# Performance work log

Hardware: AMD Instinct MI355X
Metric: run time of the kernel (lower is better)

## Reference

```python
import jax, jax.numpy as jnp
import numpy as np

B, T, D, H, O = 1024, 512, 64, 64, 32


def setup_inputs() -> dict:
    key = jax.random.key(0)
    ks = jax.random.split(key, 12)
    s = 1.0 / np.sqrt(H)  # torch LSTM/Linear default init scale
    u = lambda k, shape: jax.random.uniform(k, shape, jnp.float32, -s, s)
    return {
        "x": jax.random.normal(ks[0], (B, T, D), jnp.float32),
        # layer 0 (PyTorch gate order: i, f, g, o stacked along first dim)
        "w_ih0": u(ks[1], (4 * H, D)),
        "w_hh0": u(ks[2], (4 * H, H)),
        "b_ih0": u(ks[3], (4 * H,)),
        "b_hh0": u(ks[4], (4 * H,)),
        # layer 1
        "w_ih1": u(ks[5], (4 * H, H)),
        "w_hh1": u(ks[6], (4 * H, H)),
        "b_ih1": u(ks[7], (4 * H,)),
        "b_hh1": u(ks[8], (4 * H,)),
        # final linear head
        "fc_w": u(ks[9], (O, H)),
        "fc_b": u(ks[10], (O,)),
    }


def lstm_layer(x, w_ih, w_hh, b_ih, b_hh):
    """Single batch-first LSTM layer, PyTorch gate order (i, f, g, o)."""
    Bb = x.shape[0]
    Hh = w_hh.shape[1]
    # precompute input contribution for all timesteps: (B, T, 4H)
    pre = jnp.einsum('btd,gd->btg', x, w_ih) + b_ih + b_hh

    def step(carry, p_t):  # p_t: (B, 4H)
        h, c = carry
        gates = p_t + h @ w_hh.T
        i, f, g, o = jnp.split(gates, 4, axis=-1)
        c = jax.nn.sigmoid(f) * c + jax.nn.sigmoid(i) * jnp.tanh(g)
        h = jax.nn.sigmoid(o) * jnp.tanh(c)
        return (h, c), h

    h0 = jnp.zeros((Bb, Hh), x.dtype)
    (_, _), hs = jax.lax.scan(step, (h0, h0), jnp.swapaxes(pre, 0, 1))
    return jnp.swapaxes(hs, 0, 1)  # (B, T, H)


def reference(x, w_ih0, w_hh0, b_ih0, b_hh0, w_ih1, w_hh1, b_ih1, b_hh1, fc_w, fc_b):
    h1 = lstm_layer(x, w_ih0, w_hh0, b_ih0, b_hh0)
    h2 = lstm_layer(h1, w_ih1, w_hh1, b_ih1, b_hh1)
    last = h2[:, -1, :]  # (B, H)
    return jax.nn.softplus(last @ fc_w.T + fc_b)  # (B, O)
```

## Files before the change

### kernel.cpp

```cpp
#include <hip/hip_runtime.h>
#include <math.h>

#define BB 1024
#define TT 512
#define OO 32
#define MM 4
#define NBLK (BB/MM)
#define SS 8
#define NSLOT 66

typedef __attribute__((ext_vector_type(8))) short short8;
typedef __attribute__((ext_vector_type(4))) float f32x4;

#define MFMA __builtin_amdgcn_mfma_f32_16x16x32_bf16
#define LOG2E 1.4426950408889634f
#define K2    2.8853900817779268f

#define BAR() asm volatile("s_waitcnt lgkmcnt(0)\n\ts_barrier" ::: "memory")

__device__ __forceinline__ float exp2f_(float x) {
#if __has_builtin(__builtin_amdgcn_exp2f)
    return __builtin_amdgcn_exp2f(x);
#else
    float r; asm("v_exp_f32 %0, %1" : "=v"(r) : "v"(x)); return r;
#endif
}

__device__ __forceinline__ ushort f2bf(float f) {
    union { float f; unsigned u; } v; v.f = f;
    unsigned r = v.u + 0x7FFF + ((v.u >> 16) & 1);
    return (ushort)(r >> 16);
}
__device__ __forceinline__ float bf2f(ushort u) {
    union { unsigned u; float f; } v; v.u = ((unsigned)u) << 16; return v.f;
}
__device__ __forceinline__ unsigned pkbf(float a, float b) {
    union { float f; unsigned u; } x, y; x.f = a; y.f = b;
    return __builtin_amdgcn_perm(y.u + 0x8000u, x.u + 0x8000u, 0x07060302u);
}
__device__ __forceinline__ short8 pack8(const float4& a, const float4& b) {
    union { unsigned u[4]; short8 s; } r;
    r.u[0] = pkbf(a.x, a.y); r.u[1] = pkbf(a.z, a.w);
    r.u[2] = pkbf(b.x, b.y); r.u[3] = pkbf(b.z, b.w);
    return r.s;
}

__global__ __launch_bounds__(256, 1)
void lstm_pc(const float* __restrict__ x,
             const float* __restrict__ w_ih0,
             const float* __restrict__ w_hh0,
             const float* __restrict__ b_ih0,
             const float* __restrict__ b_hh0,
             const float* __restrict__ w_ih1,
             const float* __restrict__ w_hh1,
             const float* __restrict__ b_ih1,
             const float* __restrict__ b_hh1,
             const float* __restrict__ fc_w,
             const float* __restrict__ fc_b,
             float* __restrict__ out)
{
    __shared__ float  pre0[2][SS][4][4][64];
    __shared__ float  pre1[2][SS][4][4][64];
    __shared__ ushort h0u[16][4][80];
    __shared__ ushort h1u[2][4][80];

    const int tid = threadIdx.x;
    const int wv  = tid >> 6;
    const int ln  = tid & 63;
    const int l   = ln & 15;
    const int q   = ln >> 4;
    const int b0  = blockIdx.x * MM;
    const f32x4 z4 = (f32x4){0.f, 0.f, 0.f, 0.f};

    for (int i = tid; i < 16 * 4 * 80; i += 256) ((ushort*)h0u)[i] = 0;
    for (int i = tid; i < 2 * 4 * 80;  i += 256) ((ushort*)h1u)[i] = 0;

    if (wv < 2) {
        const float* whh = wv ? w_hh1 : w_hh0;
        short8 bf[4][4][2];
#pragma unroll
        for (int g = 0; g < 4; ++g) {
            const float sc = (g == 2) ? K2 : -LOG2E;
#pragma unroll
            for (int c = 0; c < 4; ++c) {
                const int col = 64 * g + 16 * c + l;
#pragma unroll
                for (int kt = 0; kt < 2; ++kt) {
                    const float* src = whh + col * 64 + 32 * kt + 8 * q;
                    const float4 v0 = *(const float4*)src;
                    const float4 v1 = *(const float4*)(src + 4);
                    short8 b;
                    b[0] = (short)f2bf(v0.x * sc); b[1] = (short)f2bf(v0.y * sc);
                    b[2] = (short)f2bf(v0.z * sc); b[3] = (short)f2bf(v0.w * sc);
                    b[4] = (short)f2bf(v1.x * sc); b[5] = (short)f2bf(v1.y * sc);
                    b[6] = (short)f2bf(v1.z * sc); b[7] = (short)f2bf(v1.w * sc);
                    bf[g][c][kt] = b;
                }
            }
        }
        float cc[4] = {0.f, 0.f, 0.f, 0.f};
        const int hrow = l >> 2;
        const int hsw  = (16 * q) ^ (16 * hrow);
        const float* preBase = wv ? &pre1[0][0][0][0][0] : &pre0[0][0][0][0][0];
        char* ring = (char*)(wv ? (void*)h1u : (void*)h0u);
        const int mask = wv ? 1 : 15;

        for (int s = 0; s < NSLOT; ++s) {
            BAR();
            const bool act = wv ? (s >= 2) : (s < 64);
            if (act) {
                const int u_  = wv ? (s - 2) : s;
                const int base_t = SS * u_;
                const float* pb0 = preBase + (u_ & 1) * 8192 + q * 256;
#pragma unroll
                for (int tau = 0; tau < SS; ++tau) {
                    const int t = base_t + tau;
                    const char* hb = ring + ((t - 1) & mask) * 640 + hrow * 160;
                    const short8 a0 = *(const short8*)(hb + hsw);
                    const short8 a1 = *(const short8*)(hb + 64 + hsw);
                    const float* pp = pb0 + tau * 1024;
                    float y[4][4];
#pragma unroll
                    for (int g = 0; g < 4; ++g)
#pragma unroll
                        for (int w = 0; w < 4; ++w)
                            y[g][w] = pp[g * 64 + ((16 * w + l) ^ (16 * q))];
#pragma unroll
                    for (int c = 0; c < 4; ++c)
#pragma unroll
                        for (int g = 0; g < 4; ++g) {
                            f32x4 acc = MFMA(a1, bf[g][c][1],
                                             MFMA(a0, bf[g][c][0], z4, 0, 0, 0),
                                             0, 0, 0);
                            y[g][c] += acc[0];
                        }
                    char* wb = ring + (t & mask) * 640 + q * 160;
#pragma unroll
                    for (int w = 0; w < 4; ++w) {
                        const float y0 = y[0][w], y1 = y[1][w];
                        const float y2 = y[2][w], y3 = y[3][w];
                        const float Ef = exp2f_(y1);
                        const float Ei = exp2f_(y0);
                        const float Eg = exp2f_(fminf(y2, 80.f));
                        const float sf = __builtin_amdgcn_rcpf(1.f + Ef);
                        const float rd = __builtin_amdgcn_rcpf((1.f + Ei) * (1.f + Eg));
                        cc[w] = sf * cc[w] + (Eg - 1.f) * rd;
                        const float Ec = exp2f_(fminf(cc[w] * K2, 80.f));
                        const float Eo = exp2f_(y3);
                        const float r2 = __builtin_amdgcn_rcpf((1.f + Eo) * (1.f + Ec));
                        union { float f; unsigned u; } hv; hv.f = (Ec - 1.f) * r2;
                        const ushort hval = (ushort)((hv.u + 0x8000u) >> 16);
                        *(ushort*)(wb + ((32 * w + 2 * l) ^ (16 * q))) = hval;
                    }
                }
            }
        }
    } else {
        const int c0 = 2 * (wv - 2);
        short8 wi0[4][2][2], wi1[4][2][2];
        float  bv0[4][2], bv1[4][2];
#pragma unroll
        for (int g = 0; g < 4; ++g) {
            const float sc = (g == 2) ? K2 : -LOG2E;
#pragma unroll
            for (int ci = 0; ci < 2; ++ci) {
                const int col = 64 * g + 16 * (c0 + ci) + l;
                bv0[g][ci] = (b_ih0[col] + b_hh0[col]) * sc;
                bv1[g][ci] = (b_ih1[col] + b_hh1[col]) * sc;
#pragma unroll
                for (int kt = 0; kt < 2; ++kt) {
                    const int ko = 32 * kt + 8 * q;
#define LDW(dst, W)                                                           \
                    { const float4 v0 = *(const float4*)(W + col * 64 + ko);  \
                      const float4 v1 = *(const float4*)(W + col * 64 + ko + 4); \
                      short8 b;                                               \
                      b[0]=(short)f2bf(v0.x*sc); b[1]=(short)f2bf(v0.y*sc);   \
                      b[2]=(short)f2bf(v0.z*sc); b[3]=(short)f2bf(v0.w*sc);   \
                      b[4]=(short)f2bf(v1.x*sc); b[5]=(short)f2bf(v1.y*sc);   \
                      b[6]=(short)f2bf(v1.z*sc); b[7]=(short)f2bf(v1.w*sc);   \
                      dst = b; }
                    LDW(wi0[g][ci][kt], w_ih0)
                    LDW(wi1[g][ci][kt], w_ih1)
#undef LDW
                }
            }
        }
        const int xrow = l & 3, xtau = l >> 2;
        const size_t xbase = ((size_t)(b0 + xrow) * TT) * 64 + 8 * q;

#define COOP_PRE0(S_)                                                         \
        {                                                                     \
            const int buf = ((S_) + 1) & 1;                                   \
            const int t0 = SS * ((S_) + 1);                                   \
            float* dst0 = &pre0[buf][0][0][0][0];                             \
            _Pragma("unroll")                                                 \
            for (int hh = 0; hh < 2; ++hh) {                                  \
                const float* px = x + xbase + (size_t)(t0 + 4 * hh + xtau) * 64; \
                const float4 v0 = *(const float4*)px;                         \
                const float4 v1 = *(const float4*)(px + 4);                   \
                const float4 v2 = *(const float4*)(px + 32);                  \
                const float4 v3 = *(const float4*)(px + 36);                  \
                const short8 xa0 = pack8(v0, v1), xa1 = pack8(v2, v3);        \
                _Pragma("unroll")                                             \
                for (int ci = 0; ci < 2; ++ci)                                \
                    _Pragma("unroll")                                         \
                    for (int g = 0; g < 4; ++g) {                             \
                        const float bv_ = bv0[g][ci];                         \
                        f32x4 acc = (f32x4){bv_, bv_, bv_, bv_};              \
                        acc = MFMA(xa0, wi0[g][ci][0], acc, 0, 0, 0);         \
                        acc = MFMA(xa1, wi0[g][ci][1], acc, 0, 0, 0);         \
                        const int uu = 16 * (c0 + ci) + l;                    \
                        float* dd = dst0 + (4 * hh + q) * 1024 + g * 64;      \
                        dd[0 * 256 + (uu ^ 0)]  = acc[0];                     \
                        dd[1 * 256 + (uu ^ 16)] = acc[1];                     \
                        dd[2 * 256 + (uu ^ 32)] = acc[2];                     \
                        dd[3 * 256 + (uu ^ 48)] = acc[3];                     \
                    }                                                         \
            }                                                                 \
        }

#define COOP_PRE1(S_)                                                         \
        {                                                                     \
            const int buf = ((S_) - 1) & 1;                                   \
            const int t1 = SS * ((S_) - 1);                                   \
            float* dst1 = &pre1[buf][0][0][0][0];                             \
            const int sw2 = (16 * q) ^ (16 * xrow);                           \
            _Pragma("unroll")                                                 \
            for (int hh = 0; hh < 2; ++hh) {                                  \
                const int tt = t1 + 4 * hh + xtau;                            \
                const char* hp = (const char*)h0u + (tt & 15) * 640 + xrow * 160; \
                const short8 ha0 = *(const short8*)(hp + sw2);                \
                const short8 ha1 = *(const short8*)(hp + 64 + sw2);           \
                _Pragma("unroll")                                             \
                for (int ci = 0; ci < 2; ++ci)                                \
                    _Pragma("unroll")                                         \
                    for (int g = 0; g < 4; ++g) {                             \
                        const float bv_ = bv1[g][ci];                         \
                        f32x4 acc = (f32x4){bv_, bv_, bv_, bv_};              \
                        acc = MFMA(ha0, wi1[g][ci][0], acc, 0, 0, 0);         \
                        acc = MFMA(ha1, wi1[g][ci][1], acc, 0, 0, 0);         \
                        const int uu = 16 * (c0 + ci) + l;                    \
                        float* dd = dst1 + (4 * hh + q) * 1024 + g * 64;      \
                        dd[0 * 256 + (uu ^ 0)]  = acc[0];                     \
                        dd[1 * 256 + (uu ^ 16)] = acc[1];                     \
                        dd[2 * 256 + (uu ^ 32)] = acc[2];                     \
                        dd[3 * 256 + (uu ^ 48)] = acc[3];                     \
                    }                                                         \
            }                                                                 \
        }

        COOP_PRE0(-1)
        for (int s = 0; s < NSLOT; ++s) {
            BAR();
            if (s < 63) COOP_PRE0(s)
            if (s >= 1 && s <= 64) COOP_PRE1(s)
        }
#undef COOP_PRE0
#undef COOP_PRE1
    }

    BAR();
    if (tid < MM * OO) {
        const int row = tid >> 5, o = tid & 31;
        float a = fc_b[o];
#pragma unroll
        for (int j = 0; j < 64; ++j) {
            const ushort hv = *(const ushort*)((const char*)h1u + 640
                              + row * 160 + ((2 * j) ^ (16 * row)));
            a = fmaf(fc_w[o * 64 + j], bf2f(hv), a);
        }
        out[(size_t)(b0 + row) * OO + o] =
            fmaxf(a, 0.0f) + log1pf(__expf(-fabsf(a)));
    }
}

extern "C" void kernel_launch(void* const* d_in, const int* in_sizes, int n_in,
                              void* d_out, int out_size, void* d_ws, size_t ws_size,
                              hipStream_t stream) {
    const float* x     = (const float*)d_in[0];
    const float* w_ih0 = (const float*)d_in[1];
    const float* w_hh0 = (const float*)d_in[2];
    const float* b_ih0 = (const float*)d_in[3];
    const float* b_hh0 = (const float*)d_in[4];
    const float* w_ih1 = (const float*)d_in[5];
    const float* w_hh1 = (const float*)d_in[6];
    const float* b_ih1 = (const float*)d_in[7];
    const float* b_hh1 = (const float*)d_in[8];
    const float* fc_w  = (const float*)d_in[9];
    const float* fc_b  = (const float*)d_in[10];
    float* out = (float*)d_out;

    lstm_pc<<<dim3(NBLK), dim3(256), 0, stream>>>(
        x, w_ih0, w_hh0, b_ih0, b_hh0,
        w_ih1, w_hh1, b_ih1, b_hh1, fc_w, fc_b, out);
}
```

Before: 472.9 us.

## Split each LSTM layer's recurrence across two waves and interleave input projections

Reworks the wave specialisation. Before, one wave per layer ran the whole recurrence while two waves computed the input projections. Now each layer's recurrent step is split across two waves (half the hidden columns each), and all four waves share the projection work, spread across the per-timestep tau slots. x is staged into LDS with asynchronous global_load_lds, and the pre-activation and hidden-state LDS layouts are changed for vector reads. This shortens the serial per-step critical path, at the cost of a workgroup barrier on every timestep instead of every 8 steps.

```diff
diff --git a/kernel.cpp b/kernel.cpp
--- a/kernel.cpp
+++ b/kernel.cpp
@@ -16,7 +16,8 @@
 #define LOG2E 1.4426950408889634f
 #define K2    2.8853900817779268f
 
-#define BAR() asm volatile("s_waitcnt lgkmcnt(0)\n\ts_barrier" ::: "memory")
+#define BAR()  asm volatile("s_waitcnt lgkmcnt(0)\n\ts_barrier" ::: "memory")
+#define BARV() asm volatile("s_waitcnt vmcnt(0) lgkmcnt(0)\n\ts_barrier" ::: "memory")
 
 __device__ __forceinline__ float exp2f_(float x) {
 #if __has_builtin(__builtin_amdgcn_exp2f)
@@ -45,8 +46,14 @@
     return r.s;
 }
 
+__device__ __forceinline__ void gll16(const float* g, void* l) {
+    __builtin_amdgcn_global_load_lds(
+        (const __attribute__((address_space(1))) void*)g,
+        (__attribute__((address_space(3))) void*)l, 16, 0, 0);
+}
+
 __global__ __launch_bounds__(256, 1)
-void lstm_pc(const float* __restrict__ x,
+void lstm_tw(const float* __restrict__ x,
              const float* __restrict__ w_ih0,
              const float* __restrict__ w_hh0,
              const float* __restrict__ b_ih0,
@@ -59,205 +66,259 @@
              const float* __restrict__ fc_b,
              float* __restrict__ out)
 {
-    __shared__ float  pre0[2][SS][4][4][64];
-    __shared__ float  pre1[2][SS][4][4][64];
-    __shared__ ushort h0u[16][4][80];
-    __shared__ ushort h1u[2][4][80];
+    __shared__ __align__(16) float  pre0s[2][SS][64][4][4];
+    __shared__ __align__(16) float  pre1s[2][SS][64][4][4];
+    __shared__ __align__(16) ushort h0s[16][4][64];
+    __shared__ __align__(16) ushort h1s[2][4][64];
+    __shared__ __align__(16) float  xs[2][4][SS][64];
 
     const int tid = threadIdx.x;
     const int wv  = tid >> 6;
+    const int lay = wv >> 1;
+    const int cA  = 2 * (wv & 1);
     const int ln  = tid & 63;
     const int l   = ln & 15;
     const int q   = ln >> 4;
     const int b0  = blockIdx.x * MM;
     const f32x4 z4 = (f32x4){0.f, 0.f, 0.f, 0.f};
 
-    for (int i = tid; i < 16 * 4 * 80; i += 256) ((ushort*)h0u)[i] = 0;
-    for (int i = tid; i < 2 * 4 * 80;  i += 256) ((ushort*)h1u)[i] = 0;
-
-    if (wv < 2) {
-        const float* whh = wv ? w_hh1 : w_hh0;
-        short8 bf[4][4][2];
-#pragma unroll
-        for (int g = 0; g < 4; ++g) {
-            const float sc = (g == 2) ? K2 : -LOG2E;
-#pragma unroll
-            for (int c = 0; c < 4; ++c) {
-                const int col = 64 * g + 16 * c + l;
-#pragma unroll
-                for (int kt = 0; kt < 2; ++kt) {
-                    const float* src = whh + col * 64 + 32 * kt + 8 * q;
-                    const float4 v0 = *(const float4*)src;
-                    const float4 v1 = *(const float4*)(src + 4);
-                    short8 b;
-                    b[0] = (short)f2bf(v0.x * sc); b[1] = (short)f2bf(v0.y * sc);
-                    b[2] = (short)f2bf(v0.z * sc); b[3] = (short)f2bf(v0.w * sc);
-                    b[4] = (short)f2bf(v1.x * sc); b[5] = (short)f2bf(v1.y * sc);
-                    b[6] = (short)f2bf(v1.z * sc); b[7] = (short)f2bf(v1.w * sc);
-                    bf[g][c][kt] = b;
-                }
-            }
-        }
-        float cc[4] = {0.f, 0.f, 0.f, 0.f};
-        const int hrow = l >> 2;
-        const int hsw  = (16 * q) ^ (16 * hrow);
-        const float* preBase = wv ? &pre1[0][0][0][0][0] : &pre0[0][0][0][0][0];
-        char* ring = (char*)(wv ? (void*)h1u : (void*)h0u);
-        const int mask = wv ? 1 : 15;
-
-        for (int s = 0; s < NSLOT; ++s) {
-            BAR();
-            const bool act = wv ? (s >= 2) : (s < 64);
-            if (act) {
-                const int u_  = wv ? (s - 2) : s;
-                const int base_t = SS * u_;
-                const float* pb0 = preBase + (u_ & 1) * 8192 + q * 256;
-#pragma unroll
-                for (int tau = 0; tau < SS; ++tau) {
-                    const int t = base_t + tau;
-                    const char* hb = ring + ((t - 1) & mask) * 640 + hrow * 160;
-                    const short8 a0 = *(const short8*)(hb + hsw);
-                    const short8 a1 = *(const short8*)(hb + 64 + hsw);
-                    const float* pp = pb0 + tau * 1024;
-                    float y[4][4];
+    const float* whh = lay ? w_hh1 : w_hh0;
+    short8 bf[4][2][2];
+#pragma unroll
+    for (int g = 0; g < 4; ++g) {
+        const float sc = (g == 2) ? K2 : -LOG2E;
+#pragma unroll
+        for (int ci = 0; ci < 2; ++ci) {
+            const int col = 64 * g + 16 * (cA + ci) + l;
+#pragma unroll
+            for (int kt = 0; kt < 2; ++kt) {
+                const float* src = whh + col * 64 + 32 * kt + 8 * q;
+                const float4 v0 = *(const float4*)src;
+                const float4 v1 = *(const float4*)(src + 4);
+                short8 b;
+                b[0] = (short)f2bf(v0.x * sc); b[1] = (short)f2bf(v0.y * sc);
+                b[2] = (short)f2bf(v0.z * sc); b[3] = (short)f2bf(v0.w * sc);
+                b[4] = (short)f2bf(v1.x * sc); b[5] = (short)f2bf(v1.y * sc);
+                b[6] = (short)f2bf(v1.z * sc); b[7] = (short)f2bf(v1.w * sc);
+                bf[g][ci][kt] = b;
+            }
+        }
+    }
+
+    const float scw = (wv == 2) ? K2 : -LOG2E;
+    short8 wi0[4][2], wi1[4][2];
+    float  bv0[4], bv1[4];
+#pragma unroll
+    for (int j = 0; j < 4; ++j) {
+        const int col = 64 * wv + 16 * j + l;
+        bv0[j] = (b_ih0[col] + b_hh0[col]) * scw;
+        bv1[j] = (b_ih1[col] + b_hh1[col]) * scw;
+#pragma unroll
+        for (int kt = 0; kt < 2; ++kt) {
+            const int ko = 32 * kt + 8 * q;
+#define LDW(dst, W)                                                           \
+            { const float4 v0 = *(const float4*)(W + col * 64 + ko);          \
+              const float4 v1 = *(const float4*)(W + col * 64 + ko + 4);      \
+              short8 b;                                                       \
+              b[0]=(short)f2bf(v0.x*scw); b[1]=(short)f2bf(v0.y*scw);         \
+              b[2]=(short)f2bf(v0.z*scw); b[3]=(short)f2bf(v0.w*scw);         \
+              b[4]=(short)f2bf(v1.x*scw); b[5]=(short)f2bf(v1.y*scw);         \
+              b[6]=(short)f2bf(v1.z*scw); b[7]=(short)f2bf(v1.w*scw);         \
+              dst = b; }
+            LDW(wi0[j][kt], w_ih0)
+            LDW(wi1[j][kt], w_ih1)
+#undef LDW
+        }
+    }
+
+    for (int i = tid; i < 16 * 4 * 64; i += 256) ((ushort*)h0s)[i] = 0;
+    for (int i = tid; i < 2 * 4 * 64;  i += 256) ((ushort*)h1s)[i] = 0;
+
+#pragma unroll
+    for (int c = 0; c < 2; ++c)
+#pragma unroll
+        for (int k = 0; k < 2; ++k) {
+            const int th = 4 * k;
+            const float* sr = x + (((size_t)(b0 + wv) * TT + 8 * c + th + (ln >> 4)) * 64
+                                   + (ln & 15) * 4);
+            gll16(sr, (char*)xs + c * 8192 + wv * 2048 + th * 256);
+        }
+    BARV();
+    {
+#pragma unroll
+        for (int mt = 0; mt < 2; ++mt) {
+            const float* xp = (const float*)xs + (l & 3) * 512
+                              + ((l >> 2) + 4 * mt) * 64 + 8 * q;
+            const float4 v0 = *(const float4*)xp;
+            const float4 v1 = *(const float4*)(xp + 4);
+            const float4 v2 = *(const float4*)(xp + 32);
+            const float4 v3 = *(const float4*)(xp + 36);
+            const short8 xa0 = pack8(v0, v1);
+            const short8 xa1 = pack8(v2, v3);
+            char* wp = (char*)pre0s + (q + 4 * mt) * 4096;
+#pragma unroll
+            for (int j = 0; j < 4; ++j) {
+                f32x4 a = (f32x4){bv0[j], bv0[j], bv0[j], bv0[j]};
+                a = MFMA(xa0, wi0[j][0], a, 0, 0, 0);
+                a = MFMA(xa1, wi0[j][1], a, 0, 0, 0);
+                char* wpp = wp + (16 * j + l) * 64 + wv * 4;
+#pragma unroll
+                for (int ri = 0; ri < 4; ++ri)
+                    *(float*)(wpp + ((ri * 16) ^ (q << 4))) = a[ri];
+            }
+        }
+    }
+    BAR();
+
+    float cc0 = 0.f, cc1 = 0.f;
+
+#define CELL(CCV, Y0, Y1, Y2, Y3, HVAL)                                       \
+    {                                                                         \
+        const float Ef = exp2f_(Y1);                                          \
+        const float Ei = exp2f_(Y0);                                          \
+        const float Eg = exp2f_(fminf((Y2), 80.f));                           \
+        const float sf = __builtin_amdgcn_rcpf(1.f + Ef);                     \
+        const float rd = __builtin_amdgcn_rcpf((1.f + Ei) * (1.f + Eg));      \
+        CCV = sf * CCV + (Eg - 1.f) * rd;                                     \
+        const float Ec = exp2f_(fminf(CCV * K2, 80.f));                       \
+        const float Eo = exp2f_(Y3);                                          \
+        const float r2 = __builtin_amdgcn_rcpf((1.f + Eo) * (1.f + Ec));      \
+        union { float f; unsigned u; } hv_; hv_.f = (Ec - 1.f) * r2;          \
+        HVAL = (ushort)((hv_.u + 0x8000u) >> 16);                             \
+    }
+
+    for (int s = 0; s < NSLOT; ++s) {
+        const int pb   = s & 1;
+        const bool doA = (lay == 0) && (s < 64);
+        const bool doB = (lay == 1) && (s >= 2);
+        const bool cp0 = (s <= 62);
+        const bool cp1 = (s >= 1 && s <= 64);
+        const int t0   = doA ? (8 * s) : (8 * (s - 2));
+        const int t1C  = 8 * (s - 1);
+        short8 ca0 = {0,0,0,0,0,0,0,0}, ca1 = {0,0,0,0,0,0,0,0};
+
+#pragma unroll
+        for (int tau = 0; tau < SS; ++tau) {
+            if (tau == 0) { BARV(); } else { BAR(); }
+
+            short8 a0, a1; f32x4 pv0, pv1;
+            if (doA || doB) {
+                const int t  = t0 + tau;
+                const int hm = doA ? 15 : 1;
+                const int r  = l >> 2;
+                const char* hb = (doA ? (const char*)h0s : (const char*)h1s)
+                                 + ((t - 1) & hm) * 512 + r * 128;
+                a0 = *(const short8*)(hb + ((16 * q) ^ (r << 4)));
+                a1 = *(const short8*)(hb + ((64 + 16 * q) ^ (r << 4)));
+                const char* pr = (doA ? (const char*)pre0s : (const char*)pre1s)
+                                 + pb * 16384 + tau * 4096
+                                 + ((16 * q) ^ ((tau & 3) << 4));
+                pv0 = *(const f32x4*)(pr + (16 * cA + l) * 64);
+                pv1 = *(const f32x4*)(pr + (16 * cA + 16 + l) * 64);
+            }
+
+            if (tau == 0 && s <= 61) {
+                const int sg = s + 2;
+                char* xd = (char*)xs + (sg & 1) * 8192 + wv * 2048;
+#pragma unroll
+                for (int k = 0; k < 2; ++k) {
+                    const int th = 4 * k;
+                    const float* sr = x + (((size_t)(b0 + wv) * TT + 8 * sg + th
+                                            + (ln >> 4)) * 64 + (ln & 15) * 4);
+                    gll16(sr, xd + th * 256);
+                }
+            }
+
+            if (tau < 4) {
+                if (cp0) {
+                    const int mt = tau >> 1;
+                    if ((tau & 1) == 0) {
+                        const float* xp = (const float*)xs + (pb ^ 1) * 2048
+                                          + (l & 3) * 512
+                                          + ((l >> 2) + 4 * mt) * 64 + 8 * q;
+                        const float4 v0 = *(const float4*)xp;
+                        const float4 v1 = *(const float4*)(xp + 4);
+                        const float4 v2 = *(const float4*)(xp + 32);
+                        const float4 v3 = *(const float4*)(xp + 36);
+                        ca0 = pack8(v0, v1); ca1 = pack8(v2, v3);
+                    }
+                    const int j0 = 2 * (tau & 1);
+                    char* wp = (char*)pre0s + (pb ^ 1) * 16384 + (q + 4 * mt) * 4096;
+#pragma unroll
+                    for (int jj = 0; jj < 2; ++jj) {
+                        const int j = j0 + jj;
+                        f32x4 a = (f32x4){bv0[j], bv0[j], bv0[j], bv0[j]};
+                        a = MFMA(ca0, wi0[j][0], a, 0, 0, 0);
+                        a = MFMA(ca1, wi0[j][1], a, 0, 0, 0);
+                        char* wpp = wp + (16 * j + l) * 64 + wv * 4;
+#pragma unroll
+                        for (int ri = 0; ri < 4; ++ri)
+                            *(float*)(wpp + ((ri * 16) ^ (q << 4))) = a[ri];
+                    }
+                }
+            } else {
+                if (cp1) {
+                    const int mt = (tau - 4) >> 1;
+                    if ((tau & 1) == 0) {
+                        const int tt = t1C + (l >> 2) + 4 * mt;
+                        const int rr = l & 3;
+                        const char* hp = (const char*)h0s + (tt & 15) * 512 + rr * 128;
+                        ca0 = *(const short8*)(hp + ((16 * q) ^ (rr << 4)));
+                        ca1 = *(const short8*)(hp + ((64 + 16 * q) ^ (rr << 4)));
+                    }
+                    const int j0 = 2 * (tau & 1);
+                    char* wp = (char*)pre1s + (pb ^ 1) * 16384 + (q + 4 * mt) * 4096;
+#pragma unroll
+                    for (int jj = 0; jj < 2; ++jj) {
+                        const int j = j0 + jj;
+                        f32x4 a = (f32x4){bv1[j], bv1[j], bv1[j], bv1[j]};
+                        a = MFMA(ca0, wi1[j][0], a, 0, 0, 0);
+                        a = MFMA(ca1, wi1[j][1], a, 0, 0, 0);
+                        char* wpp = wp + (16 * j + l) * 64 + wv * 4;
+#pragma unroll
+                        for (int ri = 0; ri < 4; ++ri)
+                            *(float*)(wpp + ((ri * 16) ^ (q << 4))) = a[ri];
+                    }
+                }
+            }
+
+            if (doA || doB) {
+                f32x4 acc[2][4];
+#pragma unroll
+                for (int ci = 0; ci < 2; ++ci)
 #pragma unroll
                     for (int g = 0; g < 4; ++g)
-#pragma unroll
-                        for (int w = 0; w < 4; ++w)
-                            y[g][w] = pp[g * 64 + ((16 * w + l) ^ (16 * q))];
-#pragma unroll
-                    for (int c = 0; c < 4; ++c)
-#pragma unroll
-                        for (int g = 0; g < 4; ++g) {
-                            f32x4 acc = MFMA(a1, bf[g][c][1],
-                                             MFMA(a0, bf[g][c][0], z4, 0, 0, 0),
-                                             0, 0, 0);
-                            y[g][c] += acc[0];
-                        }
-                    char* wb = ring + (t & mask) * 640 + q * 160;
-#pragma unroll
-                    for (int w = 0; w < 4; ++w) {
-                        const float y0 = y[0][w], y1 = y[1][w];
-                        const float y2 = y[2][w], y3 = y[3][w];
-                        const float Ef = exp2f_(y1);
-                        const float Ei = exp2f_(y0);
-                        const float Eg = exp2f_(fminf(y2, 80.f));
-                        const float sf = __builtin_amdgcn_rcpf(1.f + Ef);
-                        const float rd = __builtin_amdgcn_rcpf((1.f + Ei) * (1.f + Eg));
-                        cc[w] = sf * cc[w] + (Eg - 1.f) * rd;
-                        const float Ec = exp2f_(fminf(cc[w] * K2, 80.f));
-                        const float Eo = exp2f_(y3);
-                        const float r2 = __builtin_amdgcn_rcpf((1.f + Eo) * (1.f + Ec));
-                        union { float f; unsigned u; } hv; hv.f = (Ec - 1.f) * r2;
-                        const ushort hval = (ushort)((hv.u + 0x8000u) >> 16);
-                        *(ushort*)(wb + ((32 * w + 2 * l) ^ (16 * q))) = hval;
-                    }
-                }
-            }
-        }
-    } else {
-        const int c0 = 2 * (wv - 2);
-        short8 wi0[4][2][2], wi1[4][2][2];
-        float  bv0[4][2], bv1[4][2];
-#pragma unroll
-        for (int g = 0; g < 4; ++g) {
-            const float sc = (g == 2) ? K2 : -LOG2E;
-#pragma unroll
-            for (int ci = 0; ci < 2; ++ci) {
-                const int col = 64 * g + 16 * (c0 + ci) + l;
-                bv0[g][ci] = (b_ih0[col] + b_hh0[col]) * sc;
-                bv1[g][ci] = (b_ih1[col] + b_hh1[col]) * sc;
-#pragma unroll
-                for (int kt = 0; kt < 2; ++kt) {
-                    const int ko = 32 * kt + 8 * q;
-#define LDW(dst, W)                                                           \
-                    { const float4 v0 = *(const float4*)(W + col * 64 + ko);  \
-                      const float4 v1 = *(const float4*)(W + col * 64 + ko + 4); \
-                      short8 b;                                               \
-                      b[0]=(short)f2bf(v0.x*sc); b[1]=(short)f2bf(v0.y*sc);   \
-                      b[2]=(short)f2bf(v0.z*sc); b[3]=(short)f2bf(v0.w*sc);   \
-                      b[4]=(short)f2bf(v1.x*sc); b[5]=(short)f2bf(v1.y*sc);   \
-                      b[6]=(short)f2bf(v1.z*sc); b[7]=(short)f2bf(v1.w*sc);   \
-                      dst = b; }
-                    LDW(wi0[g][ci][kt], w_ih0)
-                    LDW(wi1[g][ci][kt], w_ih1)
-#undef LDW
-                }
-            }
-        }
-        const int xrow = l & 3, xtau = l >> 2;
-        const size_t xbase = ((size_t)(b0 + xrow) * TT) * 64 + 8 * q;
-
-#define COOP_PRE0(S_)                                                         \
-        {                                                                     \
-            const int buf = ((S_) + 1) & 1;                                   \
-            const int t0 = SS * ((S_) + 1);                                   \
-            float* dst0 = &pre0[buf][0][0][0][0];                             \
-            _Pragma("unroll")                                                 \
-            for (int hh = 0; hh < 2; ++hh) {                                  \
-                const float* px = x + xbase + (size_t)(t0 + 4 * hh + xtau) * 64; \
-                const float4 v0 = *(const float4*)px;                         \
-                const float4 v1 = *(const float4*)(px + 4);                   \
-                const float4 v2 = *(const float4*)(px + 32);                  \
-                const float4 v3 = *(const float4*)(px + 36);                  \
-                const short8 xa0 = pack8(v0, v1), xa1 = pack8(v2, v3);        \
-                _Pragma("unroll")                                             \
-                for (int ci = 0; ci < 2; ++ci)                                \
-                    _Pragma("unroll")                                         \
-                    for (int g = 0; g < 4; ++g) {                             \
-                        const float bv_ = bv0[g][ci];                         \
-                        f32x4 acc = (f32x4){bv_, bv_, bv_, bv_};              \
-                        acc = MFMA(xa0, wi0[g][ci][0], acc, 0, 0, 0);         \
-                        acc = MFMA(xa1, wi0[g][ci][1], acc, 0, 0, 0);         \
-                        const int uu = 16 * (c0 + ci) + l;                    \
-                        float* dd = dst0 + (4 * hh + q) * 1024 + g * 64;      \
-                        dd[0 * 256 + (uu ^ 0)]  = acc[0];                     \
-                        dd[1 * 256 + (uu ^ 16)] = acc[1];                     \
-                        dd[2 * 256 + (uu ^ 32)] = acc[2];                     \
-                        dd[3 * 256 + (uu ^ 48)] = acc[3];                     \
-                    }                                                         \
-            }                                                                 \
-        }
-
-#define COOP_PRE1(S_)                                                         \
-        {                                                                     \
-            const int buf = ((S_) - 1) & 1;                                   \
-            const int t1 = SS * ((S_) - 1);                                   \
-            float* dst1 = &pre1[buf][0][0][0][0];                             \
-            const int sw2 = (16 * q) ^ (16 * xrow);                           \
-            _Pragma("unroll")                                                 \
-            for (int hh = 0; hh < 2; ++hh) {                                  \
-                const int tt = t1 + 4 * hh + xtau;                            \
-                const char* hp = (const char*)h0u + (tt & 15) * 640 + xrow * 160; \
-                const short8 ha0 = *(const short8*)(hp + sw2);                \
-                const short8 ha1 = *(const short8*)(hp + 64 + sw2);           \
-                _Pragma("unroll")                                             \
-                for (int ci = 0; ci < 2; ++ci)                                \
-                    _Pragma("unroll")                                         \
-                    for (int g = 0; g < 4; ++g) {                             \
-                        const float bv_ = bv1[g][ci];                         \
-                        f32x4 acc = (f32x4){bv_, bv_, bv_, bv_};              \
-                        acc = MFMA(ha0, wi1[g][ci][0], acc, 0, 0, 0);         \
-                        acc = MFMA(ha1, wi1[g][ci][1], acc, 0, 0, 0);         \
-                        const int uu = 16 * (c0 + ci) + l;                    \
-                        float* dd = dst1 + (4 * hh + q) * 1024 + g * 64;      \
-                        dd[0 * 256 + (uu ^ 0)]  = acc[0];                     \
-                        dd[1 * 256 + (uu ^ 16)] = acc[1];                     \
-                        dd[2 * 256 + (uu ^ 32)] = acc[2];                     \
-                        dd[3 * 256 + (uu ^ 48)] = acc[3];                     \
-                    }                                                         \
-            }                                                                 \
-        }
-
-        COOP_PRE0(-1)
-        for (int s = 0; s < NSLOT; ++s) {
-            BAR();
-            if (s < 63) COOP_PRE0(s)
-            if (s >= 1 && s <= 64) COOP_PRE1(s)
-        }
-#undef COOP_PRE0
-#undef COOP_PRE1
-    }
+                        acc[ci][g] = MFMA(a0, bf[g][ci][0], z4, 0, 0, 0);
+#pragma unroll
+                for (int ci = 0; ci < 2; ++ci)
+#pragma unroll
+                    for (int g = 0; g < 4; ++g)
+                        acc[ci][g] = MFMA(a1, bf[g][ci][1], acc[ci][g], 0, 0, 0);
+
+                const int t  = t0 + tau;
+                const int hm = doA ? 15 : 1;
+                char* hw = (doA ? (char*)h0s : (char*)h1s)
+                           + (t & hm) * 512 + q * 128;
+                {
+                    const float y0 = pv0[0] + acc[0][0][0];
+                    const float y1 = pv0[1] + acc[0][1][0];
+                    const float y2 = pv0[2] + acc[0][2][0];
+                    const float y3 = pv0[3] + acc[0][3][0];
+                    ushort hval; CELL(cc0, y0, y1, y2, y3, hval)
+                    *(ushort*)(hw + ((2 * (16 * cA + l)) ^ (q << 4))) = hval;
+                }
+                {
+                    const float y0 = pv1[0] + acc[1][0][0];
+                    const float y1 = pv1[1] + acc[1][1][0];
+                    const float y2 = pv1[2] + acc[1][2][0];
+                    const float y3 = pv1[3] + acc[1][3][0];
+                    ushort hval; CELL(cc1, y0, y1, y2, y3, hval)
+                    *(ushort*)(hw + ((2 * (16 * cA + 16 + l)) ^ (q << 4))) = hval;
+                }
+            }
+        }
+    }
+#undef CELL
 
     BAR();
     if (tid < MM * OO) {
@@ -265,8 +326,8 @@
         float a = fc_b[o];
 #pragma unroll
         for (int j = 0; j < 64; ++j) {
-            const ushort hv = *(const ushort*)((const char*)h1u + 640
-                              + row * 160 + ((2 * j) ^ (16 * row)));
+            const ushort hv = *(const ushort*)((const char*)h1s + 512
+                              + row * 128 + ((2 * j) ^ (row << 4)));
             a = fmaf(fc_w[o * 64 + j], bf2f(hv), a);
         }
         out[(size_t)(b0 + row) * OO + o] =
@@ -290,7 +351,7 @@
     const float* fc_b  = (const float*)d_in[10];
     float* out = (float*)d_out;
 
-    lstm_pc<<<dim3(NBLK), dim3(256), 0, stream>>>(
+    lstm_tw<<<dim3(NBLK), dim3(256), 0, stream>>>(
         x, w_ih0, w_hh0, b_ih0, b_hh0,
         w_ih1, w_hh1, b_ih1, b_hh1, fc_w, fc_b, out);
 }
```

After: 569.5 us. +20.4%, slower.
